# Kernel optimization log

Measured on AMD Instinct MI355X. Metric: run time of the kernel, lower is better.

Reference implementation:

```python
import jax, jax.numpy as jnp
import numpy as np

B, S, D = 4, 2048, 1024

def setup_inputs() -> dict:
    key = jax.random.key(0)
    ks = jax.random.split(key, 7)
    sc = 1.0 / np.sqrt(D)
    return {
        "x": jax.random.normal(ks[0], (B, S, D), dtype=jnp.float32),
        "Wq": jax.random.normal(ks[1], (D, D), dtype=jnp.float32) * sc,
        "bq": jax.random.normal(ks[2], (D,), dtype=jnp.float32) * 0.01,
        "Wk": jax.random.normal(ks[3], (D, D), dtype=jnp.float32) * sc,
        "bk": jax.random.normal(ks[4], (D,), dtype=jnp.float32) * 0.01,
        "Wv": jax.random.normal(ks[5], (D, D), dtype=jnp.float32) * sc,
        "bv": jax.random.normal(ks[6], (D,), dtype=jnp.float32) * 0.01,
    }

def reference(x, Wq, bq, Wk, bk, Wv, bv):
    # q, k, v: [B, S, D] projections (torch Linear: x @ W^T + b; here W stored as [in, out])
    q = jnp.einsum("bsd,df->bsf", x, Wq) + bq
    k = jnp.einsum("bsd,df->bsf", x, Wk) + bk
    v = jnp.einsum("bsd,df->bsf", x, Wv) + bv
    dim = x.shape[-1]
    # scores: [B, S, S], scaled by sqrt(full d_model) as in the source
    scores = jnp.einsum("bqd,bkd->bqk", q, k) / jnp.sqrt(jnp.float32(dim)).astype(x.dtype)
    attn = jax.nn.softmax(scores, axis=-1)
    return jnp.einsum("bqk,bkd->bqd", attn, v)
```

## Files before the change

### kernel.cpp

```cpp
#include <hip/hip_runtime.h>
#include <hip/hip_bf16.h>

typedef __attribute__((ext_vector_type(8))) short bf16x8;
typedef __attribute__((ext_vector_type(4))) float f32x4;
typedef unsigned short u16;

__device__ __forceinline__ u16 f2bf(float f) {
  unsigned int u = __builtin_bit_cast(unsigned int, f);
  u += 0x7fffu + ((u >> 16) & 1u);
  return (u16)(u >> 16);
}
__device__ __forceinline__ float bf2f(unsigned int h) {
  unsigned int u = h << 16;
  return __builtin_bit_cast(float, u);
}

__device__ __forceinline__ void gload_lds16(const void* g, void* l) {
  __builtin_amdgcn_global_load_lds(
      (const __attribute__((address_space(1))) void*)g,
      (__attribute__((address_space(3))) void*)l, 16, 0, 0);
}

#define BAR() __builtin_amdgcn_s_barrier()
#define VMC(N) asm volatile("s_waitcnt vmcnt(%0)" ::"n"(N) : "memory")

template <int EPI>
__global__ __launch_bounds__(256) void gemm2s(
    const u16* __restrict__ Abase, const u16* __restrict__ Btbase,
    const float* __restrict__ bq, const float* __restrict__ bk,
    const float* __restrict__ bv, void* __restrict__ out0,
    void* __restrict__ out1, void* __restrict__ out2, int Kd, int ldc,
    long long sAz, long long sBz, long long sCz) {
  constexpr int ASZ = 16384;
  constexpr int BSZ = 16384;
  constexpr int BBASE = 2 * ASZ;
  __shared__ char lds[2 * ASZ + 3 * BSZ];

  const int tid = threadIdx.x;
  const int w = tid >> 6, l = tid & 63;
  const int wr = w >> 1, wc = w & 1;
  const int lq = l >> 4, lr = l & 15;
  const int bm = blockIdx.y * 128, bn = blockIdx.x * 128;
  const int z = blockIdx.z;
  const u16* A = Abase + (size_t)z * sAz;
  const u16* Bt = Btbase + (size_t)z * sBz;
  const int NT = Kd >> 6;

  const int kbp = ((tid & 7) ^ ((tid >> 3) & 7)) * 8;
  const int drow = tid >> 3;
  const u16* gA[4];
  const u16* gB[4];
#pragma unroll
  for (int u = 0; u < 4; ++u) {
    gA[u] = A + (size_t)(bm + u * 32 + drow) * Kd + kbp;
    gB[u] = Bt + (size_t)(bn + u * 32 + drow) * Kd + kbp;
  }

  auto stageA = [&](int kt) {
    char* d = lds + (kt & 1) * ASZ + tid * 16;
#pragma unroll
    for (int u = 0; u < 4; ++u) gload_lds16(gA[u] + kt * 64, d + u * 4096);
  };
  auto stageB = [&](int kt) {
    char* d = lds + BBASE + (kt % 3) * BSZ + tid * 16;
#pragma unroll
    for (int u = 0; u < 4; ++u) gload_lds16(gB[u] + kt * 64, d + u * 4096);
  };

  const int rA = wr * 64 + lr;
  const int rB0 = wc * 64 + lr;
  int aoff[2];
#pragma unroll
  for (int kh = 0; kh < 2; ++kh)
    aoff[kh] = rA * 128 + (((kh * 4 + lq) ^ (rA & 7)) << 4);

  f32x4 acc[4][2][2] = {};
  bf16x8 a[2][4];
  bf16x8 bb[2][2][2];

  auto rdA = [&](int kt) {
    const char* p = lds + (kt & 1) * ASZ;
#pragma unroll
    for (int kh = 0; kh < 2; ++kh)
#pragma unroll
      for (int mf = 0; mf < 4; ++mf)
        a[kh][mf] = *(const bf16x8*)(p + aoff[kh] + mf * 2048);
  };
  auto rdB = [&](int kt) {
    const char* p = lds + BBASE + (kt % 3) * BSZ;
#pragma unroll
    for (int nh = 0; nh < 2; ++nh) {
      const int rB = rB0 + nh * 32;
#pragma unroll
      for (int kh = 0; kh < 2; ++kh) {
        const int o = rB * 128 + (((kh * 4 + lq) ^ (rB & 7)) << 4);
#pragma unroll
        for (int nf = 0; nf < 2; ++nf)
          bb[nh][kh][nf] = *(const bf16x8*)(p + o + nf * 2048);
      }
    }
  };
  auto mma = [&](int kh) {
    __builtin_amdgcn_s_setprio(1);
#pragma unroll
    for (int nh = 0; nh < 2; ++nh)
#pragma unroll
      for (int mf = 0; mf < 4; ++mf)
#pragma unroll
        for (int nf = 0; nf < 2; ++nf)
          acc[mf][nh][nf] = __builtin_amdgcn_mfma_f32_16x16x32_bf16(
              a[kh][mf], bb[nh][kh][nf], acc[mf][nh][nf], 0, 0, 0);
    __builtin_amdgcn_s_setprio(0);
  };

  stageB(0);
  stageA(0);
  stageB(1);
  stageA(1);
  VMC(8);
  BAR();

  for (int t = 0; t < NT; ++t) {
    rdA(t);
    rdB(t);
    if (t + 2 < NT) stageB(t + 2);
    BAR();
    mma(0);
    if (t + 2 < NT) VMC(4); else VMC(0);
    BAR();
    if (t + 2 < NT) stageA(t + 2);
    mma(1);
  }

  if constexpr (EPI == 0) {
    const int mat = bn >> 10;
    const float sc = (mat == 0) ? 0.03125f : 1.0f;
    const float* bias = (mat == 0) ? bq : (mat == 1 ? bk : bv);
    u16* Q = (u16*)out0;
    u16* K = (u16*)out1;
    u16* V = (u16*)out2;
#pragma unroll
    for (int nh = 0; nh < 2; ++nh)
#pragma unroll
      for (int nf = 0; nf < 2; ++nf) {
        const int oc = (bn + wc * 64 + nh * 32 + nf * 16 + lr) & 1023;
        const float bb2 = bias[oc];
#pragma unroll
        for (int mf = 0; mf < 4; ++mf) {
          const int row = bm + wr * 64 + mf * 16 + lq * 4;
          if (mat < 2) {
            u16* dst = (mat == 0) ? Q : K;
#pragma unroll
            for (int e = 0; e < 4; ++e)
              dst[(size_t)(row + e) * 1024 + oc] =
                  f2bf((acc[mf][nh][nf][e] + bb2) * sc);
          } else {
            const int bz = row >> 11, sdx = row & 2047;
            ushort4 pk;
            pk.x = f2bf(acc[mf][nh][nf][0] + bb2);
            pk.y = f2bf(acc[mf][nh][nf][1] + bb2);
            pk.z = f2bf(acc[mf][nh][nf][2] + bb2);
            pk.w = f2bf(acc[mf][nh][nf][3] + bb2);
            *(ushort4*)&V[((size_t)bz * 1024 + oc) * 2048 + sdx] = pk;
          }
        }
      }
  } else if constexpr (EPI == 2) {
    u16* C = (u16*)out0 + (size_t)z * sCz;
#pragma unroll
    for (int nh = 0; nh < 2; ++nh)
#pragma unroll
      for (int nf = 0; nf < 2; ++nf) {
        const int col = bn + wc * 64 + nh * 32 + nf * 16 + lr;
#pragma unroll
        for (int mf = 0; mf < 4; ++mf) {
          const int row = bm + wr * 64 + mf * 16 + lq * 4;
#pragma unroll
          for (int e = 0; e < 4; ++e)
            C[(size_t)(row + e) * ldc + col] = f2bf(acc[mf][nh][nf][e]);
        }
      }
  } else {
    float* C = (float*)out0 + (size_t)z * sCz;
#pragma unroll
    for (int nh = 0; nh < 2; ++nh)
#pragma unroll
      for (int nf = 0; nf < 2; ++nf) {
        const int col = bn + wc * 64 + nh * 32 + nf * 16 + lr;
#pragma unroll
        for (int mf = 0; mf < 4; ++mf) {
          const int row = bm + wr * 64 + mf * 16 + lq * 4;
#pragma unroll
          for (int e = 0; e < 4; ++e)
            C[(size_t)(row + e) * ldc + col] = acc[mf][nh][nf][e];
        }
      }
  }
}

__global__ __launch_bounds__(256) void cvt_x(const float* __restrict__ in,
                                             u16* __restrict__ out) {
  const int i = blockIdx.x * 256 + threadIdx.x;
  const float4 v = ((const float4*)in)[i];
  ushort4 o;
  o.x = f2bf(v.x);
  o.y = f2bf(v.y);
  o.z = f2bf(v.z);
  o.w = f2bf(v.w);
  ((ushort4*)out)[i] = o;
}

__global__ void cvt_wt(const float* __restrict__ Wq,
                       const float* __restrict__ Wk,
                       const float* __restrict__ Wv, u16* __restrict__ Wt) {
  __shared__ float s[32][33];
  const float* W = blockIdx.z == 0 ? Wq : (blockIdx.z == 1 ? Wk : Wv);
  u16* O = Wt + (size_t)blockIdx.z * 1048576;
  const int k0 = blockIdx.y * 32, n0 = blockIdx.x * 32;
  s[threadIdx.y][threadIdx.x] =
      W[(size_t)(k0 + threadIdx.y) * 1024 + n0 + threadIdx.x];
  __syncthreads();
  O[(size_t)(n0 + threadIdx.y) * 1024 + k0 + threadIdx.x] =
      f2bf(s[threadIdx.x][threadIdx.y]);
}

__global__ __launch_bounds__(256) void softmax_rows(u16* __restrict__ SP) {
  const size_t base = ((size_t)blockIdx.y * 2048 + blockIdx.x) * 2048;
  u16* p = SP + base;
  const int t = threadIdx.x;
  __shared__ float red[4];

  uint4 u = ((const uint4*)p)[t];
  unsigned int uu[4] = {u.x, u.y, u.z, u.w};
  float f[8];
#pragma unroll
  for (int j = 0; j < 4; ++j) {
    f[2 * j] = bf2f(uu[j] & 0xffffu);
    f[2 * j + 1] = __builtin_bit_cast(float, uu[j] & 0xffff0000u);
  }
  float mx = f[0];
#pragma unroll
  for (int i = 1; i < 8; ++i) mx = fmaxf(mx, f[i]);
#pragma unroll
  for (int o = 32; o; o >>= 1) mx = fmaxf(mx, __shfl_xor(mx, o, 64));
  if ((t & 63) == 0) red[t >> 6] = mx;
  __syncthreads();
  mx = fmaxf(fmaxf(red[0], red[1]), fmaxf(red[2], red[3]));
  __syncthreads();

  float e[8];
  float sum = 0.f;
#pragma unroll
  for (int i = 0; i < 8; ++i) {
    e[i] = __expf(f[i] - mx);
    sum += e[i];
  }
#pragma unroll
  for (int o = 32; o; o >>= 1) sum += __shfl_xor(sum, o, 64);
  if ((t & 63) == 0) red[t >> 6] = sum;
  __syncthreads();
  sum = red[0] + red[1] + red[2] + red[3];
  const float inv = 1.0f / sum;

  uint4 ov;
  unsigned int w0[4];
#pragma unroll
  for (int j = 0; j < 4; ++j) {
    unsigned int lo = f2bf(e[2 * j] * inv);
    unsigned int hi = f2bf(e[2 * j + 1] * inv);
    w0[j] = lo | (hi << 16);
  }
  ov.x = w0[0];
  ov.y = w0[1];
  ov.z = w0[2];
  ov.w = w0[3];
  ((uint4*)p)[t] = ov;
}

extern "C" void kernel_launch(void* const* d_in, const int* in_sizes, int n_in,
                              void* d_out, int out_size, void* d_ws,
                              size_t ws_size, hipStream_t stream) {
  const float* x = (const float*)d_in[0];
  const float* Wq = (const float*)d_in[1];
  const float* bq = (const float*)d_in[2];
  const float* Wk = (const float*)d_in[3];
  const float* bk = (const float*)d_in[4];
  const float* Wv = (const float*)d_in[5];
  const float* bv = (const float*)d_in[6];
  float* out = (float*)d_out;
  char* ws = (char*)d_ws;

  u16* xb = (u16*)ws;
  u16* Wt = (u16*)(ws + 16777216);
  u16* Qb = (u16*)(ws + 23068672);
  u16* Kb = Qb + 8388608;
  u16* Vt = Kb + 8388608;
  u16* SP = Vt + 8388608;

  cvt_x<<<8192, 256, 0, stream>>>(x, xb);
  cvt_wt<<<dim3(32, 32, 3), dim3(32, 32), 0, stream>>>(Wq, Wk, Wv, Wt);

  gemm2s<0><<<dim3(24, 64, 1), 256, 0, stream>>>(
      xb, Wt, bq, bk, bv, Qb, Kb, Vt, 1024, 0, 0, 0, 0);

  gemm2s<2><<<dim3(16, 16, 4), 256, 0, stream>>>(
      Qb, Kb, nullptr, nullptr, nullptr, SP, nullptr, nullptr, 1024, 2048,
      2097152LL, 2097152LL, 4194304LL);

  softmax_rows<<<dim3(2048, 4), 256, 0, stream>>>(SP);

  gemm2s<3><<<dim3(8, 16, 4), 256, 0, stream>>>(
      SP, Vt, nullptr, nullptr, nullptr, out, nullptr, nullptr, 2048, 1024,
      4194304LL, 2097152LL, 2097152LL);
}
```

Measured before the change: 175.8 us.

## Fold Wq·Wkᵀ into one projection and fuse softmax exp into score GEMM

Rewrites the scores as x·(Wq Wkᵀ)·xᵀ plus a per-key bias term x·(Wk bq), so Q and K projections collapse into a single combined-weight projection. Terms that are constant across a row cancel in softmax and are dropped. The combined 1024x1024 weight is built with a split-K GEMM and a reduction/cast kernel. Softmax is fused into the score GEMM epilogue as an unnormalised exp with atomic row-sum accumulation, and the final GEMM divides by the row sums, removing the separate softmax pass. The max subtraction is dropped, which risks overflow for larger scores, and the atomics make the row sums nondeterministic.

```diff
diff --git a/kernel.cpp b/kernel.cpp
--- a/kernel.cpp
+++ b/kernel.cpp
@@ -10,10 +10,6 @@
   u += 0x7fffu + ((u >> 16) & 1u);
   return (u16)(u >> 16);
 }
-__device__ __forceinline__ float bf2f(unsigned int h) {
-  unsigned int u = h << 16;
-  return __builtin_bit_cast(float, u);
-}
 
 __device__ __forceinline__ void gload_lds16(const void* g, void* l) {
   __builtin_amdgcn_global_load_lds(
@@ -27,10 +23,10 @@
 template <int EPI>
 __global__ __launch_bounds__(256) void gemm2s(
     const u16* __restrict__ Abase, const u16* __restrict__ Btbase,
-    const float* __restrict__ bq, const float* __restrict__ bk,
-    const float* __restrict__ bv, void* __restrict__ out0,
-    void* __restrict__ out1, void* __restrict__ out2, int Kd, int ldc,
-    long long sAz, long long sBz, long long sCz) {
+    const float* __restrict__ p0, const float* __restrict__ p1,
+    const float* __restrict__ p2, void* __restrict__ out0,
+    void* __restrict__ out1, int Kd, int Kext, int ldc, long long sAz,
+    long long sBz, long long sCz) {
   constexpr int ASZ = 16384;
   constexpr int BSZ = 16384;
   constexpr int BBASE = 2 * ASZ;
@@ -44,7 +40,7 @@
   const int z = blockIdx.z;
   const u16* A = Abase + (size_t)z * sAz;
   const u16* Bt = Btbase + (size_t)z * sBz;
-  const int NT = Kd >> 6;
+  const int NT = Kext >> 6;
 
   const int kbp = ((tid & 7) ^ ((tid >> 3) & 7)) * 8;
   const int drow = tid >> 3;
@@ -132,29 +128,96 @@
     mma(1);
   }
 
-  if constexpr (EPI == 0) {
+  if constexpr (EPI == 4) {
+    u16* C = (u16*)out0 + (size_t)z * sCz;
+    const float* cc = p0 + z * 2048;
+    float* rs = (float*)p1 + z * 2048;
+    float psum[4][4] = {};
+#pragma unroll
+    for (int nh = 0; nh < 2; ++nh)
+#pragma unroll
+      for (int nf = 0; nf < 2; ++nf) {
+        const int col = bn + wc * 64 + nh * 32 + nf * 16 + lr;
+        const float cj = cc[col];
+#pragma unroll
+        for (int mf = 0; mf < 4; ++mf) {
+          const int row = bm + wr * 64 + mf * 16 + lq * 4;
+#pragma unroll
+          for (int e = 0; e < 4; ++e) {
+            const float pv = __expf((acc[mf][nh][nf][e] + cj) * 0.03125f);
+            C[(size_t)(row + e) * ldc + col] = f2bf(pv);
+            psum[mf][e] += pv;
+          }
+        }
+      }
+#pragma unroll
+    for (int off = 1; off <= 8; off <<= 1)
+#pragma unroll
+      for (int mf = 0; mf < 4; ++mf)
+#pragma unroll
+        for (int e = 0; e < 4; ++e)
+          psum[mf][e] += __shfl_xor(psum[mf][e], off, 64);
+    if (lr == 0) {
+#pragma unroll
+      for (int mf = 0; mf < 4; ++mf)
+#pragma unroll
+        for (int e = 0; e < 4; ++e)
+          atomicAdd(&rs[bm + wr * 64 + mf * 16 + lq * 4 + e], psum[mf][e]);
+    }
+  } else if constexpr (EPI == 5) {
+    float* C = (float*)out0 + (size_t)z * sCz;
+    const float* rs = p0 + z * 2048;
+#pragma unroll
+    for (int nh = 0; nh < 2; ++nh)
+#pragma unroll
+      for (int nf = 0; nf < 2; ++nf) {
+        const int col = bn + wc * 64 + nh * 32 + nf * 16 + lr;
+#pragma unroll
+        for (int mf = 0; mf < 4; ++mf) {
+          const int row = bm + wr * 64 + mf * 16 + lq * 4;
+#pragma unroll
+          for (int e = 0; e < 4; ++e)
+            C[(size_t)(row + e) * ldc + col] =
+                acc[mf][nh][nf][e] / rs[row + e];
+        }
+      }
+  } else if constexpr (EPI == 6) {
+    float* C = (float*)out0 + (size_t)z * sCz;
+#pragma unroll
+    for (int nh = 0; nh < 2; ++nh)
+#pragma unroll
+      for (int nf = 0; nf < 2; ++nf) {
+        const int col = bn + wc * 64 + nh * 32 + nf * 16 + lr;
+#pragma unroll
+        for (int mf = 0; mf < 4; ++mf) {
+          const int row = bm + wr * 64 + mf * 16 + lq * 4;
+#pragma unroll
+          for (int e = 0; e < 4; ++e)
+            C[(size_t)(row + e) * ldc + col] = acc[mf][nh][nf][e];
+        }
+      }
+  } else {
     const int mat = bn >> 10;
-    const float sc = (mat == 0) ? 0.03125f : 1.0f;
-    const float* bias = (mat == 0) ? bq : (mat == 1 ? bk : bv);
-    u16* Q = (u16*)out0;
-    u16* K = (u16*)out1;
-    u16* V = (u16*)out2;
+    u16* T = (u16*)out0;
+    u16* V = (u16*)out1;
 #pragma unroll
     for (int nh = 0; nh < 2; ++nh)
 #pragma unroll
       for (int nf = 0; nf < 2; ++nf) {
         const int oc = (bn + wc * 64 + nh * 32 + nf * 16 + lr) & 1023;
-        const float bb2 = bias[oc];
-#pragma unroll
-        for (int mf = 0; mf < 4; ++mf) {
-          const int row = bm + wr * 64 + mf * 16 + lq * 4;
-          if (mat < 2) {
-            u16* dst = (mat == 0) ? Q : K;
+        if (mat == 0) {
+#pragma unroll
+          for (int mf = 0; mf < 4; ++mf) {
+            const int row = bm + wr * 64 + mf * 16 + lq * 4;
 #pragma unroll
             for (int e = 0; e < 4; ++e)
-              dst[(size_t)(row + e) * 1024 + oc] =
-                  f2bf((acc[mf][nh][nf][e] + bb2) * sc);
-          } else {
+              T[(size_t)(row + e) * 1024 + oc] = f2bf(acc[mf][nh][nf][e]);
+          }
+        } else {
+          const float bb2 = p2[oc];
+#pragma unroll
+          for (int mf = 0; mf < 4; ++mf) {
+            const int row = bm + wr * 64 + mf * 16 + lq * 4;
             const int bz = row >> 11, sdx = row & 2047;
             ushort4 pk;
             pk.x = f2bf(acc[mf][nh][nf][0] + bb2);
@@ -163,36 +226,6 @@
             pk.w = f2bf(acc[mf][nh][nf][3] + bb2);
             *(ushort4*)&V[((size_t)bz * 1024 + oc) * 2048 + sdx] = pk;
           }
-        }
-      }
-  } else if constexpr (EPI == 2) {
-    u16* C = (u16*)out0 + (size_t)z * sCz;
-#pragma unroll
-    for (int nh = 0; nh < 2; ++nh)
-#pragma unroll
-      for (int nf = 0; nf < 2; ++nf) {
-        const int col = bn + wc * 64 + nh * 32 + nf * 16 + lr;
-#pragma unroll
-        for (int mf = 0; mf < 4; ++mf) {
-          const int row = bm + wr * 64 + mf * 16 + lq * 4;
-#pragma unroll
-          for (int e = 0; e < 4; ++e)
-            C[(size_t)(row + e) * ldc + col] = f2bf(acc[mf][nh][nf][e]);
-        }
-      }
-  } else {
-    float* C = (float*)out0 + (size_t)z * sCz;
-#pragma unroll
-    for (int nh = 0; nh < 2; ++nh)
-#pragma unroll
-      for (int nf = 0; nf < 2; ++nf) {
-        const int col = bn + wc * 64 + nh * 32 + nf * 16 + lr;
-#pragma unroll
-        for (int mf = 0; mf < 4; ++mf) {
-          const int row = bm + wr * 64 + mf * 16 + lq * 4;
-#pragma unroll
-          for (int e = 0; e < 4; ++e)
-            C[(size_t)(row + e) * ldc + col] = acc[mf][nh][nf][e];
         }
       }
   }
@@ -210,71 +243,72 @@
   ((ushort4*)out)[i] = o;
 }
 
-__global__ void cvt_wt(const float* __restrict__ Wq,
+__global__ void cvt_w3(const float* __restrict__ Wq,
                        const float* __restrict__ Wk,
-                       const float* __restrict__ Wv, u16* __restrict__ Wt) {
+                       const float* __restrict__ Wv, u16* __restrict__ Wqb,
+                       u16* __restrict__ Wkb, u16* __restrict__ WtTV) {
   __shared__ float s[32][33];
-  const float* W = blockIdx.z == 0 ? Wq : (blockIdx.z == 1 ? Wk : Wv);
-  u16* O = Wt + (size_t)blockIdx.z * 1048576;
+  const int tx = threadIdx.x, ty = threadIdx.y;
   const int k0 = blockIdx.y * 32, n0 = blockIdx.x * 32;
-  s[threadIdx.y][threadIdx.x] =
-      W[(size_t)(k0 + threadIdx.y) * 1024 + n0 + threadIdx.x];
+  if (blockIdx.z == 2) {
+    s[ty][tx] = Wv[(size_t)(k0 + ty) * 1024 + n0 + tx];
+    __syncthreads();
+    WtTV[1048576 + (size_t)(n0 + ty) * 1024 + k0 + tx] = f2bf(s[tx][ty]);
+  } else {
+    const float* W = blockIdx.z ? Wk : Wq;
+    u16* O = blockIdx.z ? Wkb : Wqb;
+    const size_t i = (size_t)(k0 + ty) * 1024 + n0 + tx;
+    O[i] = f2bf(W[i]);
+  }
+}
+
+__global__ __launch_bounds__(256) void mcast(const float* __restrict__ Mf,
+                                             u16* __restrict__ Mt) {
+  const int i = blockIdx.x * 256 + threadIdx.x;
+  const float4 a = ((const float4*)Mf)[i];
+  const float4 b = ((const float4*)(Mf + 1048576))[i];
+  const float4 c = ((const float4*)(Mf + 2097152))[i];
+  const float4 d = ((const float4*)(Mf + 3145728))[i];
+  ushort4 o;
+  o.x = f2bf(a.x + b.x + c.x + d.x);
+  o.y = f2bf(a.y + b.y + c.y + d.y);
+  o.z = f2bf(a.z + b.z + c.z + d.z);
+  o.w = f2bf(a.w + b.w + c.w + d.w);
+  ((ushort4*)Mt)[i] = o;
+}
+
+__global__ __launch_bounds__(256) void vker(const float* __restrict__ Wk,
+                                            const float* __restrict__ bq,
+                                            float* __restrict__ v) {
+  const int d = blockIdx.x, t = threadIdx.x;
+  const float4 wv = ((const float4*)(Wk + (size_t)d * 1024))[t];
+  const float4 bv = ((const float4*)bq)[t];
+  float p = wv.x * bv.x + wv.y * bv.y + wv.z * bv.z + wv.w * bv.w;
+#pragma unroll
+  for (int o = 32; o; o >>= 1) p += __shfl_xor(p, o, 64);
+  __shared__ float red[4];
+  if ((t & 63) == 0) red[t >> 6] = p;
   __syncthreads();
-  O[(size_t)(n0 + threadIdx.y) * 1024 + k0 + threadIdx.x] =
-      f2bf(s[threadIdx.x][threadIdx.y]);
-}
-
-__global__ __launch_bounds__(256) void softmax_rows(u16* __restrict__ SP) {
-  const size_t base = ((size_t)blockIdx.y * 2048 + blockIdx.x) * 2048;
-  u16* p = SP + base;
-  const int t = threadIdx.x;
-  __shared__ float red[4];
-
-  uint4 u = ((const uint4*)p)[t];
-  unsigned int uu[4] = {u.x, u.y, u.z, u.w};
-  float f[8];
-#pragma unroll
-  for (int j = 0; j < 4; ++j) {
-    f[2 * j] = bf2f(uu[j] & 0xffffu);
-    f[2 * j + 1] = __builtin_bit_cast(float, uu[j] & 0xffff0000u);
-  }
-  float mx = f[0];
-#pragma unroll
-  for (int i = 1; i < 8; ++i) mx = fmaxf(mx, f[i]);
-#pragma unroll
-  for (int o = 32; o; o >>= 1) mx = fmaxf(mx, __shfl_xor(mx, o, 64));
-  if ((t & 63) == 0) red[t >> 6] = mx;
-  __syncthreads();
-  mx = fmaxf(fmaxf(red[0], red[1]), fmaxf(red[2], red[3]));
-  __syncthreads();
-
-  float e[8];
-  float sum = 0.f;
-#pragma unroll
-  for (int i = 0; i < 8; ++i) {
-    e[i] = __expf(f[i] - mx);
-    sum += e[i];
-  }
-#pragma unroll
-  for (int o = 32; o; o >>= 1) sum += __shfl_xor(sum, o, 64);
-  if ((t & 63) == 0) red[t >> 6] = sum;
-  __syncthreads();
-  sum = red[0] + red[1] + red[2] + red[3];
-  const float inv = 1.0f / sum;
-
-  uint4 ov;
-  unsigned int w0[4];
-#pragma unroll
-  for (int j = 0; j < 4; ++j) {
-    unsigned int lo = f2bf(e[2 * j] * inv);
-    unsigned int hi = f2bf(e[2 * j + 1] * inv);
-    w0[j] = lo | (hi << 16);
-  }
-  ov.x = w0[0];
-  ov.y = w0[1];
-  ov.z = w0[2];
-  ov.w = w0[3];
-  ((uint4*)p)[t] = ov;
+  if (t == 0) v[d] = red[0] + red[1] + red[2] + red[3];
+}
+
+__global__ __launch_bounds__(256) void cker(const float* __restrict__ x,
+                                            const float* __restrict__ v,
+                                            float* __restrict__ c) {
+  const int j = blockIdx.x * 8 + (threadIdx.x >> 5);
+  const int lane = threadIdx.x & 31;
+  const float* xr = x + (size_t)j * 1024;
+  float p = 0.f;
+#pragma unroll
+  for (int k = 0; k < 8; ++k) {
+    const int i4 = k * 32 + lane;
+    const float4 xv = ((const float4*)xr)[i4];
+    const float4 vv = ((const float4*)v)[i4];
+    p += xv.x * vv.x + xv.y * vv.y + xv.z * vv.z + xv.w * vv.w;
+  }
+#pragma unroll
+  for (int o = 16; o; o >>= 1) p += __shfl_xor(p, o, 64);
+  if (lane == 0) c[j] = p;
 }
 
 extern "C" void kernel_launch(void* const* d_in, const int* in_sizes, int n_in,
@@ -284,32 +318,44 @@
   const float* Wq = (const float*)d_in[1];
   const float* bq = (const float*)d_in[2];
   const float* Wk = (const float*)d_in[3];
-  const float* bk = (const float*)d_in[4];
+  const float* bv = (const float*)d_in[6];
   const float* Wv = (const float*)d_in[5];
-  const float* bv = (const float*)d_in[6];
   float* out = (float*)d_out;
   char* ws = (char*)d_ws;
 
   u16* xb = (u16*)ws;
-  u16* Wt = (u16*)(ws + 16777216);
-  u16* Qb = (u16*)(ws + 23068672);
-  u16* Kb = Qb + 8388608;
-  u16* Vt = Kb + 8388608;
-  u16* SP = Vt + 8388608;
+  u16* WtTV = (u16*)(ws + 16777216);
+  u16* Wqb = (u16*)(ws + 20971520);
+  u16* Wkb = (u16*)(ws + 23068672);
+  float* vvec = (float*)(ws + 25165824);
+  float* cvec = (float*)(ws + 25169920);
+  float* rowsum = (float*)(ws + 25202688);
+  float* Mf32 = (float*)(ws + 25235456);
+  u16* T = (u16*)(ws + 25235456);
+  u16* Vt = (u16*)(ws + 42012672);
+  u16* SP = (u16*)(ws + 58789888);
+
+  hipMemsetAsync(rowsum, 0, 32768, stream);
 
   cvt_x<<<8192, 256, 0, stream>>>(x, xb);
-  cvt_wt<<<dim3(32, 32, 3), dim3(32, 32), 0, stream>>>(Wq, Wk, Wv, Wt);
-
-  gemm2s<0><<<dim3(24, 64, 1), 256, 0, stream>>>(
-      xb, Wt, bq, bk, bv, Qb, Kb, Vt, 1024, 0, 0, 0, 0);
-
-  gemm2s<2><<<dim3(16, 16, 4), 256, 0, stream>>>(
-      Qb, Kb, nullptr, nullptr, nullptr, SP, nullptr, nullptr, 1024, 2048,
-      2097152LL, 2097152LL, 4194304LL);
-
-  softmax_rows<<<dim3(2048, 4), 256, 0, stream>>>(SP);
-
-  gemm2s<3><<<dim3(8, 16, 4), 256, 0, stream>>>(
-      SP, Vt, nullptr, nullptr, nullptr, out, nullptr, nullptr, 2048, 1024,
+  cvt_w3<<<dim3(32, 32, 3), dim3(32, 32), 0, stream>>>(Wq, Wk, Wv, Wqb, Wkb,
+                                                       WtTV);
+  vker<<<1024, 256, 0, stream>>>(Wk, bq, vvec);
+  cker<<<1024, 256, 0, stream>>>(x, vvec, cvec);
+
+  gemm2s<6><<<dim3(8, 8, 4), 256, 0, stream>>>(
+      Wkb, Wqb, nullptr, nullptr, nullptr, Mf32, nullptr, 1024, 256, 1024,
+      256LL, 256LL, 1048576LL);
+  mcast<<<1024, 256, 0, stream>>>(Mf32, WtTV);
+
+  gemm2s<7><<<dim3(16, 64, 1), 256, 0, stream>>>(
+      xb, WtTV, nullptr, nullptr, bv, T, Vt, 1024, 1024, 0, 0, 0, 0);
+
+  gemm2s<4><<<dim3(16, 16, 4), 256, 0, stream>>>(
+      T, xb, cvec, rowsum, nullptr, SP, nullptr, 1024, 1024, 2048, 2097152LL,
+      2097152LL, 4194304LL);
+
+  gemm2s<5><<<dim3(8, 16, 4), 256, 0, stream>>>(
+      SP, Vt, rowsum, nullptr, nullptr, out, nullptr, 2048, 2048, 1024,
       4194304LL, 2097152LL, 2097152LL);
 }
```

Measured after the change: 181.3 us. 3.1% more time.
